# Performance work log

Hardware: AMD Instinct MI355X
Metric: run time of the kernel (lower is better)

Reference implementation:

```python
import jax, jax.numpy as jnp
import numpy as np


def setup_inputs() -> dict:
    key = jax.random.key(0)
    k1, k2 = jax.random.split(key)
    B, C, T = 64, 16, 32768
    y_pred = jax.random.normal(k1, (B, C, T), dtype=jnp.float32)
    y_true = jax.random.normal(k2, (B, C, T), dtype=jnp.float32)
    return {"y_pred": y_pred, "y_true": y_true}


def reference(y_pred, y_true):
    # Original: for i in 1..T, sum |cumsum(pred[:,:,:i]) - cumsum(true[:,:,:i])|, mean over batch.
    # Prefix position t (0-indexed) appears in all outer iterations i >= t+1, i.e. (T - t) times.
    # => total = mean_b sum_{c,t} |cumsum(pred - true)[b,c,t]| * (T - t)
    B, C, T = y_pred.shape
    c = jnp.cumsum(y_pred - y_true, axis=2)          # (B, C, T)
    w = (T - jnp.arange(T)).astype(y_pred.dtype)     # weight T-t for position t
    total = jnp.sum(jnp.abs(c) * w, axis=(1, 2))     # (B,)
    total = jnp.mean(total)
    scaling = 2.0 / (T * C * (T * C + 1))            # apply_scaling_factor=True
    return scaling * total
```

## Files before the change

kernel.cpp:

```cpp
#include <hip/hip_runtime.h>

#define B_BATCH 64
#define C_CH    16
#define T_LEN   32768
#define THREADS 512
#define NWAVE   (THREADS / 64)
#define VEC     4
#define CHUNK   (THREADS * VEC)
#define NCHUNK  (T_LEN / CHUNK)
#define NROWS   (B_BATCH * C_CH)

__global__ __launch_bounds__(THREADS, 8) void wloss_scan_kernel(
    const float* __restrict__ pred,
    const float* __restrict__ tru,
    double* __restrict__ partials)
{
    __shared__ float  s_wt[2][NWAVE];
    __shared__ double s_d[NWAVE];

    const int row  = blockIdx.x;
    const int tid  = threadIdx.x;
    const int lane = tid & 63;
    const int wave = tid >> 6;

    const float4* p4 = (const float4*)(pred + (size_t)row * T_LEN);
    const float4* t4 = (const float4*)(tru  + (size_t)row * T_LEN);

    float  carry = 0.0f;
    double acc   = 0.0;

    float4 cp = p4[tid];
    float4 ct = t4[tid];

    for (int ch = 0; ch < NCHUNK; ++ch) {
        const int nx = (ch + 1 < NCHUNK ? ch + 1 : NCHUNK - 1) * (CHUNK / VEC) + tid;
        float4 np = p4[nx];
        float4 nt = t4[nx];

        float s1 = cp.x - ct.x;
        float s2 = s1 + (cp.y - ct.y);
        float s3 = s2 + (cp.z - ct.z);
        float s4 = s3 + (cp.w - ct.w);

        float v = s4;
        #pragma unroll
        for (int off = 1; off < 64; off <<= 1) {
            float u = __shfl_up(v, off, 64);
            if (lane >= off) v += u;
        }

        const int par = ch & 1;
        if (lane == 63) s_wt[par][wave] = v;
        __syncthreads();

        float wpre = 0.0f, tot = 0.0f;
        #pragma unroll
        for (int w = 0; w < NWAVE; ++w) {
            float wt = s_wt[par][w];
            if (w < wave) wpre += wt;
            tot += wt;
        }

        const float excl = carry + wpre + (v - s4);
        const int   e0   = ch * CHUNK + tid * VEC;
        const float w0   = (float)(T_LEN - e0);
        float part = fabsf(excl + s1) *  w0
                   + fabsf(excl + s2) * (w0 - 1.0f)
                   + fabsf(excl + s3) * (w0 - 2.0f)
                   + fabsf(excl + s4) * (w0 - 3.0f);
        acc   += (double)part;
        carry += tot;

        cp = np; ct = nt;
    }

    #pragma unroll
    for (int off = 32; off > 0; off >>= 1)
        acc += __shfl_down(acc, off, 64);
    if (lane == 0) s_d[wave] = acc;
    __syncthreads();

    if (tid == 0) {
        double s = 0.0;
        #pragma unroll
        for (int w = 0; w < NWAVE; ++w) s += s_d[w];
        partials[row] = s;
    }
}

__global__ __launch_bounds__(256) void wloss_finalize_kernel(
    const double* __restrict__ partials, float* __restrict__ out)
{
    const int tid  = threadIdx.x;
    const int lane = tid & 63;
    const int wave = tid >> 6;

    double acc = 0.0;
    for (int i = tid; i < NROWS; i += 256) acc += partials[i];

    #pragma unroll
    for (int off = 32; off > 0; off >>= 1)
        acc += __shfl_down(acc, off, 64);

    __shared__ double dtot[4];
    if (lane == 0) dtot[wave] = acc;
    __syncthreads();

    if (tid == 0) {
        const double tot     = dtot[0] + dtot[1] + dtot[2] + dtot[3];
        const double tc      = (double)T_LEN * (double)C_CH;
        const double scaling = 2.0 / (tc * (tc + 1.0));
        out[0] = (float)(tot * scaling / (double)B_BATCH);
    }
}

extern "C" void kernel_launch(void* const* d_in, const int* in_sizes, int n_in,
                              void* d_out, int out_size, void* d_ws, size_t ws_size,
                              hipStream_t stream)
{
    const float* pred = (const float*)d_in[0];
    const float* tru  = (const float*)d_in[1];
    double* partials  = (double*)d_ws;
    float*  out       = (float*)d_out;

    wloss_scan_kernel    <<<NROWS, THREADS, 0, stream>>>(pred, tru, partials);
    wloss_finalize_kernel<<<1,     256,     0, stream>>>(partials, out);
}
```

Baseline: 280.3 us.

## Stage chunks into LDS with async global_load_lds double buffering

Replaces the register-prefetch of the next float4 chunk with direct global-to-LDS asynchronous loads (global_load_lds, 16 bytes per lane) into double-buffered shared arrays. Explicit s_waitcnt and raw s_barrier calls wrapped in sched_barriers replace __syncthreads to order the async copies against the scan. The aim is to take the load data path off VGPRs and let the next chunk's transfer overlap the current chunk's scan. In exchange each block now uses about 32KB of LDS, adds an LDS read per chunk, and relies on hand-placed wait counts being correct.

```diff
diff --git a/kernel.cpp b/kernel.cpp
--- a/kernel.cpp
+++ b/kernel.cpp
@@ -5,16 +5,23 @@
 #define T_LEN   32768
 #define THREADS 512
 #define NWAVE   (THREADS / 64)
-#define VEC     4
-#define CHUNK   (THREADS * VEC)
+#define CHUNK   2048
 #define NCHUNK  (T_LEN / CHUNK)
 #define NROWS   (B_BATCH * C_CH)
+
+__device__ __forceinline__ void stage16(const float* g, float* l) {
+    __builtin_amdgcn_global_load_lds(
+        (const __attribute__((address_space(1))) unsigned int*)g,
+        (__attribute__((address_space(3))) unsigned int*)l, 16, 0, 0);
+}
 
 __global__ __launch_bounds__(THREADS, 8) void wloss_scan_kernel(
     const float* __restrict__ pred,
     const float* __restrict__ tru,
     double* __restrict__ partials)
 {
+    __shared__ float  sP[2][CHUNK];
+    __shared__ float  sT[2][CHUNK];
     __shared__ float  s_wt[2][NWAVE];
     __shared__ double s_d[NWAVE];
 
@@ -23,24 +30,38 @@
     const int lane = tid & 63;
     const int wave = tid >> 6;
 
-    const float4* p4 = (const float4*)(pred + (size_t)row * T_LEN);
-    const float4* t4 = (const float4*)(tru  + (size_t)row * T_LEN);
+    const float* Pr = pred + (size_t)row * T_LEN;
+    const float* Tr = tru  + (size_t)row * T_LEN;
+
+#define STAGE(ch, b) do {                                   \
+        const int _o = (ch) * CHUNK + (tid << 2);           \
+        stage16(Pr + _o, &sP[b][wave << 8]);                \
+        stage16(Tr + _o, &sT[b][wave << 8]);                \
+    } while (0)
 
     float  carry = 0.0f;
     double acc   = 0.0;
 
-    float4 cp = p4[tid];
-    float4 ct = t4[tid];
+    STAGE(0, 0);
 
     for (int ch = 0; ch < NCHUNK; ++ch) {
-        const int nx = (ch + 1 < NCHUNK ? ch + 1 : NCHUNK - 1) * (CHUNK / VEC) + tid;
-        float4 np = p4[nx];
-        float4 nt = t4[nx];
+        const int buf = ch & 1;
+        if (ch + 1 < NCHUNK) {
+            STAGE(ch + 1, buf ^ 1);
+            asm volatile("s_waitcnt vmcnt(2)" ::: "memory");
+        } else {
+            asm volatile("s_waitcnt vmcnt(0)" ::: "memory");
+        }
+        __builtin_amdgcn_sched_barrier(0);
+        __builtin_amdgcn_s_barrier();
+        __builtin_amdgcn_sched_barrier(0);
 
-        float s1 = cp.x - ct.x;
-        float s2 = s1 + (cp.y - ct.y);
-        float s3 = s2 + (cp.z - ct.z);
-        float s4 = s3 + (cp.w - ct.w);
+        float4 p = *(const float4*)&sP[buf][tid << 2];
+        float4 t = *(const float4*)&sT[buf][tid << 2];
+        float s1 = p.x - t.x;
+        float s2 = s1 + (p.y - t.y);
+        float s3 = s2 + (p.z - t.z);
+        float s4 = s3 + (p.w - t.w);
 
         float v = s4;
         #pragma unroll
@@ -48,21 +69,23 @@
             float u = __shfl_up(v, off, 64);
             if (lane >= off) v += u;
         }
+        if (lane == 63) s_wt[buf][wave] = v;
 
-        const int par = ch & 1;
-        if (lane == 63) s_wt[par][wave] = v;
-        __syncthreads();
+        asm volatile("s_waitcnt lgkmcnt(0)" ::: "memory");
+        __builtin_amdgcn_sched_barrier(0);
+        __builtin_amdgcn_s_barrier();
+        __builtin_amdgcn_sched_barrier(0);
 
         float wpre = 0.0f, tot = 0.0f;
         #pragma unroll
         for (int w = 0; w < NWAVE; ++w) {
-            float wt = s_wt[par][w];
+            float wt = s_wt[buf][w];
             if (w < wave) wpre += wt;
             tot += wt;
         }
 
         const float excl = carry + wpre + (v - s4);
-        const int   e0   = ch * CHUNK + tid * VEC;
+        const int   e0   = ch * CHUNK + (tid << 2);
         const float w0   = (float)(T_LEN - e0);
         float part = fabsf(excl + s1) *  w0
                    + fabsf(excl + s2) * (w0 - 1.0f)
@@ -70,9 +93,8 @@
                    + fabsf(excl + s4) * (w0 - 3.0f);
         acc   += (double)part;
         carry += tot;
-
-        cp = np; ct = nt;
     }
+#undef STAGE
 
     #pragma unroll
     for (int off = 32; off > 0; off >>= 1)
```

Result: no change. 283.7 us (+1.2%).

## Scan per-wave contiguous spans in registers with a single block barrier

Applied to the files above, without the earlier changes.

Each wave now owns a contiguous 4096-element span of the row. It scans 16 slices with wave shuffles and keeps the partial sums in registers, then combines the wave totals through one shared-memory barrier before computing the weighted absolute sums in a second pass. This removes the per-chunk block barrier and serial carry chain, and issues four outstanding loads per stream to raise memory-level parallelism. In exchange it uses many more registers per thread, with launch bounds lowered to match, which can reduce occupancy.

```diff
diff --git a/kernel.cpp b/kernel.cpp
--- a/kernel.cpp
+++ b/kernel.cpp
@@ -4,18 +4,17 @@
 #define C_CH    16
 #define T_LEN   32768
 #define THREADS 512
-#define NWAVE   (THREADS / 64)
-#define VEC     4
-#define CHUNK   (THREADS * VEC)
-#define NCHUNK  (T_LEN / CHUNK)
+#define NWAVE   8
+#define WSPAN   4096
+#define NSLICE  16
 #define NROWS   (B_BATCH * C_CH)
 
-__global__ __launch_bounds__(THREADS, 8) void wloss_scan_kernel(
+__global__ __launch_bounds__(THREADS, 2) void wloss_row_kernel(
     const float* __restrict__ pred,
     const float* __restrict__ tru,
     double* __restrict__ partials)
 {
-    __shared__ float  s_wt[2][NWAVE];
+    __shared__ float  s_wt[NWAVE];
     __shared__ double s_d[NWAVE];
 
     const int row  = blockIdx.x;
@@ -23,24 +22,28 @@
     const int lane = tid & 63;
     const int wave = tid >> 6;
 
-    const float4* p4 = (const float4*)(pred + (size_t)row * T_LEN);
-    const float4* t4 = (const float4*)(tru  + (size_t)row * T_LEN);
+    const float4* P = (const float4*)(pred + (size_t)row * T_LEN + wave * WSPAN) + lane;
+    const float4* Q = (const float4*)(tru  + (size_t)row * T_LEN + wave * WSPAN) + lane;
 
-    float  carry = 0.0f;
-    double acc   = 0.0;
+    float a_[NSLICE], b_[NSLICE], c_[NSLICE], d_[NSLICE];
+    float e_[NSLICE];
+    float tot_[NSLICE];
 
-    float4 cp = p4[tid];
-    float4 ct = t4[tid];
+    float4 pb[4], tb[4];
+    #pragma unroll
+    for (int i = 0; i < 4; ++i) { pb[i] = P[i * 64]; tb[i] = Q[i * 64]; }
 
-    for (int ch = 0; ch < NCHUNK; ++ch) {
-        const int nx = (ch + 1 < NCHUNK ? ch + 1 : NCHUNK - 1) * (CHUNK / VEC) + tid;
-        float4 np = p4[nx];
-        float4 nt = t4[nx];
-
-        float s1 = cp.x - ct.x;
-        float s2 = s1 + (cp.y - ct.y);
-        float s3 = s2 + (cp.z - ct.z);
-        float s4 = s3 + (cp.w - ct.w);
+    #pragma unroll
+    for (int g = 0; g < NSLICE; ++g) {
+        float4 p = pb[g & 3], t = tb[g & 3];
+        if (g + 4 < NSLICE) {
+            pb[g & 3] = P[(g + 4) * 64];
+            tb[g & 3] = Q[(g + 4) * 64];
+        }
+        float s1 = p.x - t.x;
+        float s2 = s1 + (p.y - t.y);
+        float s3 = s2 + (p.z - t.z);
+        float s4 = s3 + (p.w - t.w);
 
         float v = s4;
         #pragma unroll
@@ -48,30 +51,36 @@
             float u = __shfl_up(v, off, 64);
             if (lane >= off) v += u;
         }
+        a_[g] = s1; b_[g] = s2; c_[g] = s3; d_[g] = s4;
+        e_[g] = v - s4;
+        tot_[g] = __shfl(v, 63, 64);
+    }
 
-        const int par = ch & 1;
-        if (lane == 63) s_wt[par][wave] = v;
-        __syncthreads();
+    float wtot = 0.f;
+    #pragma unroll
+    for (int g = 0; g < NSLICE; ++g) wtot += tot_[g];
+    if (lane == 0) s_wt[wave] = wtot;
+    __syncthreads();
 
-        float wpre = 0.0f, tot = 0.0f;
-        #pragma unroll
-        for (int w = 0; w < NWAVE; ++w) {
-            float wt = s_wt[par][w];
-            if (w < wave) wpre += wt;
-            tot += wt;
-        }
+    float run = 0.f;
+    #pragma unroll
+    for (int w = 0; w < NWAVE; ++w) {
+        float wt = s_wt[w];
+        if (w < wave) run += wt;
+    }
 
-        const float excl = carry + wpre + (v - s4);
-        const int   e0   = ch * CHUNK + tid * VEC;
+    double acc = 0.0;
+    #pragma unroll
+    for (int g = 0; g < NSLICE; ++g) {
+        const float excl = run + e_[g];
+        const int   e0   = wave * WSPAN + g * 256 + lane * 4;
         const float w0   = (float)(T_LEN - e0);
-        float part = fabsf(excl + s1) *  w0
-                   + fabsf(excl + s2) * (w0 - 1.0f)
-                   + fabsf(excl + s3) * (w0 - 2.0f)
-                   + fabsf(excl + s4) * (w0 - 3.0f);
-        acc   += (double)part;
-        carry += tot;
-
-        cp = np; ct = nt;
+        float part = fabsf(excl + a_[g]) *  w0
+                   + fabsf(excl + b_[g]) * (w0 - 1.0f)
+                   + fabsf(excl + c_[g]) * (w0 - 2.0f)
+                   + fabsf(excl + d_[g]) * (w0 - 3.0f);
+        acc += (double)part;
+        run += tot_[g];
     }
 
     #pragma unroll
@@ -123,6 +132,6 @@
     double* partials  = (double*)d_ws;
     float*  out       = (float*)d_out;
 
-    wloss_scan_kernel    <<<NROWS, THREADS, 0, stream>>>(pred, tru, partials);
+    wloss_row_kernel     <<<NROWS, THREADS, 0, stream>>>(pred, tru, partials);
     wloss_finalize_kernel<<<1,     256,     0, stream>>>(partials, out);
 }
```

After: 278.2 us. No clear change (-0.8%).
